# Performance work log

Hardware: AMD Instinct MI355X
Metric: run time of the kernel (lower is better)

Reference implementation:

```python
import jax, jax.numpy as jnp
import numpy as np

B, N, DIM, H, DH = 8, 1024, 512, 8, 64
INNER = H * DH  # 512
G = DH // 4     # SE(3) groups of size 4 per head


def setup_inputs() -> dict:
    key = jax.random.key(0)
    ks = jax.random.split(key, 6)
    x = jax.random.normal(ks[0], (B, N, DIM), jnp.float32)
    rotations = jax.random.normal(ks[1], (B, N, 3, 3), jnp.float32)
    translations = jax.random.normal(ks[2], (B, N, 3), jnp.float32)
    # JaxLinear init: trunc-normal std = 1/sqrt(fan_in), zero bias
    w_qkv = jax.random.normal(ks[3], (DIM, 3 * INNER), jnp.float32) * (1.0 / np.sqrt(DIM))
    b_qkv = jnp.zeros((3 * INNER,), jnp.float32)
    w_out = jax.random.normal(ks[4], (INNER, DIM), jnp.float32) * (1.0 / np.sqrt(INNER))
    b_out = jnp.zeros((DIM,), jnp.float32)
    return {"x": x, "rotations": rotations, "translations": translations,
            "w_qkv": w_qkv, "b_qkv": b_qkv, "w_out": w_out, "b_out": b_out}


def _apply_pose(P, t, transpose):
    # P: [B,N,4,4]; t: [B,H,N,DH] -> reshape to groups of 4 and rotate each group
    tg = t.reshape(B, H, N, G, 4)
    sub = 'bnji,bhncj->bhnci' if transpose else 'bnij,bhncj->bhnci'
    return jnp.einsum(sub, P, tg).reshape(B, H, N, DH)


def reference(x, rotations, translations, w_qkv, b_qkv, w_out, b_out):
    scale = DH ** -0.5
    qkv = x @ w_qkv + b_qkv                      # [B,N,3*INNER]
    q, k, v = jnp.split(qkv, 3, axis=-1)
    to_heads = lambda t: t.reshape(B, N, H, DH).transpose(0, 2, 1, 3)  # b n (h d) -> b h n d
    q, k, v = to_heads(q), to_heads(k), to_heads(v)

    # SE(3) pose matrices
    eye4 = jnp.eye(4, dtype=x.dtype)
    Rt = jnp.swapaxes(rotations, -1, -2)
    t_inv = -jnp.einsum('bnij,bnj->bni', Rt, translations)
    P_qinv = (jnp.broadcast_to(eye4, (B, N, 4, 4))
              .at[..., :3, :3].set(Rt)
              .at[..., :3, 3].set(t_inv))       # inverted query poses
    P_kv = (jnp.broadcast_to(eye4, (B, N, 4, 4))
            .at[..., :3, :3].set(rotations)
            .at[..., :3, 3].set(translations))  # key/value poses

    # per-token rotation of q/k/v (q uses P_qinv^T per original einsum)
    q = _apply_pose(P_qinv, q, transpose=True)
    k = _apply_pose(P_kv, k, transpose=False)
    v = _apply_pose(P_kv, v, transpose=False)   # v_transform=True

    attn = jax.nn.softmax(jnp.einsum('bhqd,bhkd->bhqk', q, k) * scale, axis=-1)
    out = jnp.einsum('bhqk,bhkd->bhqd', attn, v)
    out = _apply_pose(P_qinv, out, transpose=False)  # inverse transform on output

    out = out.transpose(0, 2, 1, 3).reshape(B, N, INNER)  # b h n d -> b n (h d)
    return out @ w_out + b_out
```

## Files before the change

### kernel.cpp

```cpp
#include <hip/hip_runtime.h>
#include <math.h>

#define BSZ   8
#define NSEQ  1024
#define DIM   512
#define NH    8
#define DH    64
#define INNER 512
#define NTOK  (BSZ*NSEQ)
#define QKVN  (3*INNER)

typedef __bf16   bf16x8 __attribute__((ext_vector_type(8)));
typedef _Float16 f16x8  __attribute__((ext_vector_type(8)));
typedef float    f32x4  __attribute__((ext_vector_type(4)));

#define QSCL (0.125f * 1.44269504088896f)

static __device__ __forceinline__ ushort f2bf(float f) {
    union { float f; unsigned u; } v; v.f = f;
    unsigned r = (v.u + 0x7FFFu + ((v.u >> 16) & 1u)) >> 16;
    return (ushort)r;
}
static __device__ __forceinline__ ushort f2h(float f) {
    _Float16 h = (_Float16)f;
    return __builtin_bit_cast(unsigned short, h);
}
static __device__ __forceinline__ void async16(const void* g, void* l) {
    __builtin_amdgcn_global_load_lds(
        (const __attribute__((address_space(1))) unsigned int*)g,
        (__attribute__((address_space(3))) unsigned int*)l, 16, 0, 0);
}

__global__ __launch_bounds__(256) void prep_kernel(
    const float* __restrict__ x,  ushort* __restrict__ xf,
    const float* __restrict__ wq, ushort* __restrict__ wqT,
    const float* __restrict__ wo, ushort* __restrict__ woT)
{
    const int bid = blockIdx.x;
    if (bid < 4096) {
        const int i = bid*256 + threadIdx.x;
        float4 v = ((const float4*)x)[i];
        ushort4 h = { f2h(v.x), f2h(v.y), f2h(v.z), f2h(v.w) };
        ((ushort4*)xf)[i] = h;
        return;
    }
    __shared__ float tile[32][33];
    int K, F, bx, by; const float* in; ushort* outp; int is_q;
    if (bid < 4096 + 768) {
        const int id = bid - 4096;
        bx = id % 48; by = id / 48;
        K = DIM; F = QKVN; in = wq; outp = wqT; is_q = 1;
    } else {
        const int id = bid - 4864;
        bx = id % 16; by = id / 16;
        K = INNER; F = DIM; in = wo; outp = woT; is_q = 0;
    }
    const int lx = threadIdx.x & 31, ly = threadIdx.x >> 5;
#pragma unroll
    for (int u = 0; u < 4; u++) {
        const int k = by*32 + ly + u*8;
        tile[ly + u*8][lx] = in[(size_t)k*F + bx*32 + lx];
    }
    __syncthreads();
#pragma unroll
    for (int u = 0; u < 4; u++) {
        const int f = bx*32 + ly + u*8;
        const float v = tile[lx][ly + u*8];
        outp[(size_t)f*K + by*32 + lx] = is_q ? f2h(v) : f2bf(v);
    }
}

__global__ __launch_bounds__(256) void qkv_gemm_f16(
    const ushort* __restrict__ Ag,
    const ushort* __restrict__ Bg,
    const float* __restrict__ bias, const float* __restrict__ rot,
    const float* __restrict__ trans,
    ushort* __restrict__ qb, ushort* __restrict__ kb, ushort* __restrict__ vt)
{
    extern __shared__ __align__(16) char smem[];

    const int tid  = threadIdx.x;
    const int lane = tid & 63;
    const int w    = tid >> 6;
    const int c    = lane & 15;
    const int quad = lane >> 4;
    const int wr   = w >> 1, wc = w & 1;
    const int tn   = blockIdx.x;
    const int tf   = blockIdx.y;

    f32x4 acc[4][4] = {};

    const int part = w >> 1;
    const int g0   = (w & 1) * 4;
    const ushort* src = (part == 0) ? Ag : Bg;
    const ushort* wbase = src + (size_t)((part == 0 ? tf : tn)*128 + g0*16 + c)*DIM
                          + quad*8;

    auto stage = [&](int k0, int buf) {
#pragma unroll
        for (int g = 0; g < 4; g++)
            async16(wbase + (size_t)g*16*DIM + k0,
                    smem + buf*16384 + part*8192 + (g0 + g)*1024);
    };

    stage(0, 0);
    stage(32, 1);

    for (int ch = 0; ch < 16; ch++) {
        const int cur = ch % 3;
        if (ch < 15) {
            __asm__ volatile("s_waitcnt vmcnt(4)\n\ts_barrier" ::: "memory");
        } else {
            __asm__ volatile("s_waitcnt vmcnt(0)\n\ts_barrier" ::: "memory");
        }
        if (ch < 14) stage((ch+2)*32, (ch+2) % 3);

        const char* B = smem + cur*16384;
        f16x8 fa[4], fb[4];
#pragma unroll
        for (int i = 0; i < 4; i++)
            fa[i] = *(const f16x8*)(B + (wr*4 + i)*1024 + lane*16);
#pragma unroll
        for (int j = 0; j < 4; j++)
            fb[j] = *(const f16x8*)(B + 8192 + (wc*4 + j)*1024 + lane*16);
#pragma unroll
        for (int i = 0; i < 4; i++)
#pragma unroll
            for (int j = 0; j < 4; j++)
                acc[i][j] = __builtin_amdgcn_mfma_f32_16x16x32_f16(
                    fa[i], fb[j], acc[i][j], 0, 0, 0);
    }

    const int sec = tf >> 2;

#pragma unroll
    for (int j = 0; j < 4; j++) {
        const int tc = tn*128 + wc*64 + j*16 + c;
        const int bb = tc >> 10, n = tc & 1023;
        const float* R = rot   + (size_t)(bb*NSEQ + n)*9;
        const float* T = trans + (size_t)(bb*NSEQ + n)*3;
        const float R0=R[0],R1=R[1],R2=R[2],R3=R[3],R4=R[4],R5=R[5],R6=R[6],R7=R[7],R8=R[8];
        const float T0=T[0],T1=T[1],T2=T[2];
        float ti0 = 0.f, ti1 = 0.f, ti2 = 0.f;
        if (sec == 0) {
            ti0 = -(R0*T0 + R3*T1 + R6*T2);
            ti1 = -(R1*T0 + R4*T1 + R7*T2);
            ti2 = -(R2*T0 + R5*T1 + R8*T2);
        }
#pragma unroll
        for (int i = 0; i < 4; i++) {
            const int fr = tf*128 + wr*64 + i*16 + quad*4;
            const int fl = fr & 511;
            const int h  = fl >> 6, d = fl & 63;
            float4 bv = *(const float4*)(bias + fr);
            const float g0v = acc[i][j][0] + bv.x;
            const float g1v = acc[i][j][1] + bv.y;
            const float g2v = acc[i][j][2] + bv.z;
            const float g3v = acc[i][j][3] + bv.w;
            if (sec == 0) {
                float o0 = (R0*g0v + R1*g1v + R2*g2v) * QSCL;
                float o1 = (R3*g0v + R4*g1v + R5*g2v) * QSCL;
                float o2 = (R6*g0v + R7*g1v + R8*g2v) * QSCL;
                float o3 = (ti0*g0v + ti1*g1v + ti2*g2v + g3v) * QSCL;
                ushort4 ov = { f2bf(o0), f2bf(o1), f2bf(o2), f2bf(o3) };
                *(ushort4*)(qb + ((size_t)((bb*NH + h)*NSEQ + n))*DH + d) = ov;
            } else {
                float o0 = R0*g0v + R1*g1v + R2*g2v + T0*g3v;
                float o1 = R3*g0v + R4*g1v + R5*g2v + T1*g3v;
                float o2 = R6*g0v + R7*g1v + R8*g2v + T2*g3v;
                float o3 = g3v;
                if (sec == 1) {
                    ushort4 ov = { f2bf(o0), f2bf(o1), f2bf(o2), f2bf(o3) };
                    *(ushort4*)(kb + ((size_t)((bb*NH + h)*NSEQ + n))*DH + d) = ov;
                } else {
                    ushort* vtb = vt + ((size_t)(bb*NH + h)*DH + d)*NSEQ + n;
                    vtb[0*NSEQ] = f2bf(o0);
                    vtb[1*NSEQ] = f2bf(o1);
                    vtb[2*NSEQ] = f2bf(o2);
                    vtb[3*NSEQ] = f2bf(o3);
                }
            }
        }
    }
}

__global__ __launch_bounds__(256, 2) void attn_mfma_kernel(
    const ushort* __restrict__ qb, const ushort* __restrict__ kb,
    const ushort* __restrict__ vt, const float* __restrict__ rot,
    const float* __restrict__ trans, ushort* __restrict__ om)
{
    __shared__ __align__(16) char smem[58368];

    const int tid  = threadIdx.x;
    const int lane = tid & 63;
    const int w    = tid >> 6;
    const int c    = lane & 15;
    const int quad = lane >> 4;

    const int o   = blockIdx.x;
    const int wid = (o & 7) * 128 + (o >> 3);
    const int qt  = wid & 15;
    const int bh  = wid >> 4;
    const int bb = bh >> 3, h = bh & 7;

    const ushort* Q = qb + (size_t)bh * NSEQ * DH;
    const ushort* K = kb + (size_t)bh * NSEQ * DH;
    const ushort* V = vt + (size_t)bh * DH * NSEQ;

    bf16x8 qf[2];
    {
        const ushort* qrow = Q + (size_t)(qt*64 + w*16 + c)*DH + quad*8;
        qf[0] = *(const bf16x8*)(qrow);
        qf[1] = *(const bf16x8*)(qrow + 32);
    }

    f32x4 Oacc[4] = {};
    float lsum[4] = {};

    auto stage = [&](int kt, int buf) {
#pragma unroll
        for (int u = 0; u < 2; u++) {
            const int seg = w + u*4;
            const int nt = seg >> 1, hh = seg & 1;
            const ushort* g = K + (size_t)(kt*64 + nt*16 + c)*DH + hh*32 + quad*8;
            async16(g, smem + buf*16384 + seg*1024);
        }
#pragma unroll
        for (int u = 0; u < 2; u++) {
            const int s2 = w + u*4;
            const int nt = s2 >> 1, kc = s2 & 1;
            const ushort* g = V + (size_t)(nt*16 + c)*NSEQ + kt*64 + kc*32 + quad*8;
            async16(g, smem + buf*16384 + 8192 + s2*1024);
        }
    };

    stage(0, 0);
    stage(1, 1);

    ushort (*Psw)[72] = (ushort (*)[72])(smem + 49152 + w*2304);

    for (int kt = 0; kt < 16; kt++) {
        const int cur = kt % 3;
        if (kt < 15) {
            __asm__ volatile("s_waitcnt vmcnt(4)\n\ts_barrier" ::: "memory");
        } else {
            __asm__ volatile("s_waitcnt vmcnt(0)\n\ts_barrier" ::: "memory");
        }
        if (kt < 14) stage(kt + 2, (kt + 2) % 3);

        const char* Kb = smem + cur*16384;
        const char* Vb = smem + cur*16384 + 8192;

        f32x4 s[4];
#pragma unroll
        for (int nt = 0; nt < 4; nt++) {
            bf16x8 k0 = *(const bf16x8*)(Kb + (nt*2+0)*1024 + lane*16);
            bf16x8 k1 = *(const bf16x8*)(Kb + (nt*2+1)*1024 + lane*16);
            f32x4 a = {0.f, 0.f, 0.f, 0.f};
            a = __builtin_amdgcn_mfma_f32_16x16x32_bf16(qf[0], k0, a, 0, 0, 0);
            a = __builtin_amdgcn_mfma_f32_16x16x32_bf16(qf[1], k1, a, 0, 0, 0);
            s[nt] = a;
        }

#pragma unroll
        for (int nt = 0; nt < 4; nt++)
#pragma unroll
            for (int r = 0; r < 4; r++) {
                const float p = exp2f(s[nt][r]);
                lsum[r] += p;
                Psw[quad*4 + r][nt*16 + c] = (ushort)__builtin_bit_cast(
                    unsigned short, (__bf16)p);
            }
        __asm__ volatile("s_waitcnt lgkmcnt(0)" ::: "memory");

#pragma unroll
        for (int kc2 = 0; kc2 < 2; kc2++) {
            bf16x8 vfr[4];
#pragma unroll
            for (int nt = 0; nt < 4; nt++)
                vfr[nt] = *(const bf16x8*)(Vb + (nt*2+kc2)*1024 + lane*16);
            bf16x8 a = *(const bf16x8*)&Psw[c][kc2*32 + quad*8];
#pragma unroll
            for (int nt = 0; nt < 4; nt++)
                Oacc[nt] = __builtin_amdgcn_mfma_f32_16x16x32_bf16(
                    a, vfr[nt], Oacc[nt], 0, 0, 0);
        }
    }

#pragma unroll
    for (int mk = 1; mk < 16; mk <<= 1)
#pragma unroll
        for (int r = 0; r < 4; r++)
            lsum[r] += __shfl_xor(lsum[r], mk);

    __syncthreads();
    float (*Osh)[68] = (float (*)[68])smem;
    {
        float inv[4];
#pragma unroll
        for (int r = 0; r < 4; r++) inv[r] = 1.f / lsum[r];
#pragma unroll
        for (int nt = 0; nt < 4; nt++)
#pragma unroll
            for (int r = 0; r < 4; r++)
                Osh[w*16 + quad*4 + r][nt*16 + c] = Oacc[nt][r] * inv[r];
    }
    __syncthreads();

#pragma unroll
    for (int u = 0; u < 4; u++) {
        const int t   = tid + u*256;
        const int row = t >> 4;
        const int g   = t & 15;
        const int n   = qt*64 + row;
        const float o0 = Osh[row][g*4+0], o1 = Osh[row][g*4+1];
        const float o2 = Osh[row][g*4+2], o3 = Osh[row][g*4+3];
        const float* R = rot   + (size_t)(bb*NSEQ + n)*9;
        const float* T = trans + (size_t)(bb*NSEQ + n)*3;
        const float ti0 = -(R[0]*T[0] + R[3]*T[1] + R[6]*T[2]);
        const float ti1 = -(R[1]*T[0] + R[4]*T[1] + R[7]*T[2]);
        const float ti2 = -(R[2]*T[0] + R[5]*T[1] + R[8]*T[2]);
        const float p0 = R[0]*o0 + R[3]*o1 + R[6]*o2 + ti0*o3;
        const float p1 = R[1]*o0 + R[4]*o1 + R[7]*o2 + ti1*o3;
        const float p2 = R[2]*o0 + R[5]*o1 + R[8]*o2 + ti2*o3;
        const float p3 = o3;
        ushort4 hv = { f2bf(p0), f2bf(p1), f2bf(p2), f2bf(p3) };
        *(ushort4*)(om + (size_t)(bb*NSEQ + n)*INNER + h*DH + g*4) = hv;
    }
}

__global__ __launch_bounds__(256) void out_gemm_mfma(
    const ushort* __restrict__ Ag, const ushort* __restrict__ Bg,
    const float* __restrict__ bias, float* __restrict__ out)
{
    extern __shared__ __align__(16) char smem[];

    const int tid  = threadIdx.x;
    const int lane = tid & 63;
    const int w    = tid >> 6;
    const int c    = lane & 15;
    const int quad = lane >> 4;
    const int wr   = w >> 1, wc = w & 1;
    const int tn   = blockIdx.x;
    const int tf   = blockIdx.y;

    f32x4 acc[4][4] = {};

    const int part = w >> 1;
    const int g0   = (w & 1) * 4;
    const ushort* src = (part == 0) ? Ag : Bg;
    const ushort* wbase = src + (size_t)((part == 0 ? tf : tn)*128 + g0*16 + c)*INNER
                          + quad*8;

    auto stage = [&](int k0, int buf) {
#pragma unroll
        for (int g = 0; g < 4; g++)
            async16(wbase + (size_t)g*16*INNER + k0,
                    smem + buf*16384 + part*8192 + (g0 + g)*1024);
    };

    stage(0, 0);
    stage(32, 1);
    stage(64, 2);

    for (int ch = 0; ch < 16; ch++) {
        const int cur = ch & 3;
        if (ch < 14) {
            __asm__ volatile("s_waitcnt vmcnt(8)\n\ts_barrier" ::: "memory");
        } else if (ch == 14) {
            __asm__ volatile("s_waitcnt vmcnt(4)\n\ts_barrier" ::: "memory");
        } else {
            __asm__ volatile("s_waitcnt vmcnt(0)\n\ts_barrier" ::: "memory");
        }
        if (ch < 13) stage((ch+3)*32, (ch+3) & 3);

        const char* B = smem + cur*16384;
        bf16x8 fa[4], fb[4];
#pragma unroll
        for (int i = 0; i < 4; i++)
            fa[i] = *(const bf16x8*)(B + (wr*4 + i)*1024 + lane*16);
#pragma unroll
        for (int j = 0; j < 4; j++)
            fb[j] = *(const bf16x8*)(B + 8192 + (wc*4 + j)*1024 + lane*16);
#pragma unroll
        for (int i = 0; i < 4; i++)
#pragma unroll
            for (int j = 0; j < 4; j++)
                acc[i][j] = __builtin_amdgcn_mfma_f32_16x16x32_bf16(
                    fa[i], fb[j], acc[i][j], 0, 0, 0);
    }

#pragma unroll
    for (int j = 0; j < 4; j++) {
        const int tc = tn*128 + wc*64 + j*16 + c;
#pragma unroll
        for (int i = 0; i < 4; i++) {
            const int fr = tf*128 + wr*64 + i*16 + quad*4;
            float4 bv = *(const float4*)(bias + fr);
            float4 ov = { acc[i][j][0] + bv.x, acc[i][j][1] + bv.y,
                          acc[i][j][2] + bv.z, acc[i][j][3] + bv.w };
            *(float4*)(out + (size_t)tc*DIM + fr) = ov;
        }
    }
}

extern "C" void kernel_launch(void* const* d_in, const int* in_sizes, int n_in,
                              void* d_out, int out_size, void* d_ws, size_t ws_size,
                              hipStream_t stream) {
    (void)in_sizes; (void)n_in; (void)out_size; (void)ws_size;
    const float* x     = (const float*)d_in[0];
    const float* rot   = (const float*)d_in[1];
    const float* trans = (const float*)d_in[2];
    const float* w_qkv = (const float*)d_in[3];
    const float* b_qkv = (const float*)d_in[4];
    const float* w_out = (const float*)d_in[5];
    const float* b_out = (const float*)d_in[6];
    float* out = (float*)d_out;

    const size_t HB = (size_t)BSZ*NH*NSEQ*DH;
    ushort* qb   = (ushort*)d_ws;
    ushort* kb   = qb   + HB;
    ushort* vt   = kb   + HB;
    ushort* woTh = vt   + HB;
    ushort* wqTh = woTh + (size_t)DIM*INNER;
    ushort* xf   = wqTh + (size_t)QKVN*DIM;
    ushort* om   = xf;

    static int s_attr_done = 0;
    if (!s_attr_done) {
        (void)hipFuncSetAttribute((const void*)out_gemm_mfma,
            hipFuncAttributeMaxDynamicSharedMemorySize, 65536);
        s_attr_done = 1;
    }

    prep_kernel<<<dim3(5120), 256, 0, stream>>>(
        x, xf, w_qkv, wqTh, w_out, woTh);

    qkv_gemm_f16<<<dim3(NTOK/128, QKVN/128), 256, 49152, stream>>>(
        wqTh, xf, b_qkv, rot, trans, qb, kb, vt);
    attn_mfma_kernel<<<dim3(1024), 256, 0, stream>>>(
        qb, kb, vt, rot, trans, om);
    out_gemm_mfma<<<dim3(NTOK/128, DIM/128), 256, 65536, stream>>>(
        woTh, om, b_out, out);
}
```

Before: 168.4 us.

## Shrink GEMM shared-memory footprints to raise occupancy; halve out-GEMM feature tile

The QKV GEMM drops from a 3-stage to a 2-stage LDS ring (32KB instead of 48KB) and adds an extra barrier after each chunk's MFMAs so a buffer is not overwritten while still being read. The output GEMM now uses 64x128 tiles with 2x4 accumulators per wave, which doubles the grid. It keeps a 4-deep ring of 12KB stages (48KB total), removes the dynamic-shared-memory attribute call, and adds launch_bounds(…,2). The aim is more resident blocks per CU and better latency hiding. The costs are less prefetch depth, an extra barrier per iteration in the QKV GEMM, and more redundant B-tile loads in the output GEMM.

```diff
diff --git a/kernel.cpp b/kernel.cpp
--- a/kernel.cpp
+++ b/kernel.cpp
@@ -104,16 +104,15 @@
     };
 
     stage(0, 0);
-    stage(32, 1);
 
     for (int ch = 0; ch < 16; ch++) {
-        const int cur = ch % 3;
+        const int cur = ch & 1, nxt = cur ^ 1;
         if (ch < 15) {
+            stage((ch+1)*32, nxt);
             __asm__ volatile("s_waitcnt vmcnt(4)\n\ts_barrier" ::: "memory");
         } else {
             __asm__ volatile("s_waitcnt vmcnt(0)\n\ts_barrier" ::: "memory");
         }
-        if (ch < 14) stage((ch+2)*32, (ch+2) % 3);
 
         const char* B = smem + cur*16384;
         f16x8 fa[4], fb[4];
@@ -129,6 +128,7 @@
             for (int j = 0; j < 4; j++)
                 acc[i][j] = __builtin_amdgcn_mfma_f32_16x16x32_f16(
                     fa[i], fb[j], acc[i][j], 0, 0, 0);
+        __asm__ volatile("s_waitcnt lgkmcnt(0)\n\ts_barrier" ::: "memory");
     }
 
     const int sec = tf >> 2;
@@ -329,7 +329,7 @@
     }
 }
 
-__global__ __launch_bounds__(256) void out_gemm_mfma(
+__global__ __launch_bounds__(256, 2) void out_gemm_mfma(
     const ushort* __restrict__ Ag, const ushort* __restrict__ Bg,
     const float* __restrict__ bias, float* __restrict__ out)
 {
@@ -344,19 +344,23 @@
     const int tn   = blockIdx.x;
     const int tf   = blockIdx.y;
 
-    f32x4 acc[4][4] = {};
-
-    const int part = w >> 1;
-    const int g0   = (w & 1) * 4;
-    const ushort* src = (part == 0) ? Ag : Bg;
-    const ushort* wbase = src + (size_t)((part == 0 ? tf : tn)*128 + g0*16 + c)*INNER
-                          + quad*8;
+    f32x4 acc[2][4] = {};
 
     auto stage = [&](int k0, int buf) {
 #pragma unroll
-        for (int g = 0; g < 4; g++)
-            async16(wbase + (size_t)g*16*INNER + k0,
-                    smem + buf*16384 + part*8192 + (g0 + g)*1024);
+        for (int g = 0; g < 3; g++) {
+            const int s = w*3 + g;
+            const ushort* src;
+            int dst;
+            if (s < 4) {
+                src = Ag + (size_t)(tf*64 + s*16 + c)*INNER + k0 + quad*8;
+                dst = buf*12288 + s*1024;
+            } else {
+                src = Bg + (size_t)(tn*128 + (s-4)*16 + c)*INNER + k0 + quad*8;
+                dst = buf*12288 + 4096 + (s-4)*1024;
+            }
+            async16(src, smem + dst);
+        }
     };
 
     stage(0, 0);
@@ -365,25 +369,25 @@
 
     for (int ch = 0; ch < 16; ch++) {
         const int cur = ch & 3;
-        if (ch < 14) {
-            __asm__ volatile("s_waitcnt vmcnt(8)\n\ts_barrier" ::: "memory");
+        if (ch <= 13) {
+            __asm__ volatile("s_waitcnt vmcnt(6)\n\ts_barrier" ::: "memory");
         } else if (ch == 14) {
-            __asm__ volatile("s_waitcnt vmcnt(4)\n\ts_barrier" ::: "memory");
+            __asm__ volatile("s_waitcnt vmcnt(3)\n\ts_barrier" ::: "memory");
         } else {
             __asm__ volatile("s_waitcnt vmcnt(0)\n\ts_barrier" ::: "memory");
         }
         if (ch < 13) stage((ch+3)*32, (ch+3) & 3);
 
-        const char* B = smem + cur*16384;
-        bf16x8 fa[4], fb[4];
-#pragma unroll
-        for (int i = 0; i < 4; i++)
-            fa[i] = *(const bf16x8*)(B + (wr*4 + i)*1024 + lane*16);
+        const char* B = smem + cur*12288;
+        bf16x8 fa[2], fb[4];
+#pragma unroll
+        for (int i = 0; i < 2; i++)
+            fa[i] = *(const bf16x8*)(B + (wr*2 + i)*1024 + lane*16);
 #pragma unroll
         for (int j = 0; j < 4; j++)
-            fb[j] = *(const bf16x8*)(B + 8192 + (wc*4 + j)*1024 + lane*16);
-#pragma unroll
-        for (int i = 0; i < 4; i++)
+            fb[j] = *(const bf16x8*)(B + 4096 + (wc*4 + j)*1024 + lane*16);
+#pragma unroll
+        for (int i = 0; i < 2; i++)
 #pragma unroll
             for (int j = 0; j < 4; j++)
                 acc[i][j] = __builtin_amdgcn_mfma_f32_16x16x32_bf16(
@@ -394,8 +398,8 @@
     for (int j = 0; j < 4; j++) {
         const int tc = tn*128 + wc*64 + j*16 + c;
 #pragma unroll
-        for (int i = 0; i < 4; i++) {
-            const int fr = tf*128 + wr*64 + i*16 + quad*4;
+        for (int i = 0; i < 2; i++) {
+            const int fr = tf*64 + wr*32 + i*16 + quad*4;
             float4 bv = *(const float4*)(bias + fr);
             float4 ov = { acc[i][j][0] + bv.x, acc[i][j][1] + bv.y,
                           acc[i][j][2] + bv.z, acc[i][j][3] + bv.w };
@@ -426,20 +430,13 @@
     ushort* xf   = wqTh + (size_t)QKVN*DIM;
     ushort* om   = xf;
 
-    static int s_attr_done = 0;
-    if (!s_attr_done) {
-        (void)hipFuncSetAttribute((const void*)out_gemm_mfma,
-            hipFuncAttributeMaxDynamicSharedMemorySize, 65536);
-        s_attr_done = 1;
-    }
-
     prep_kernel<<<dim3(5120), 256, 0, stream>>>(
         x, xf, w_qkv, wqTh, w_out, woTh);
 
-    qkv_gemm_f16<<<dim3(NTOK/128, QKVN/128), 256, 49152, stream>>>(
+    qkv_gemm_f16<<<dim3(NTOK/128, QKVN/128), 256, 32768, stream>>>(
         wqTh, xf, b_qkv, rot, trans, qb, kb, vt);
     attn_mfma_kernel<<<dim3(1024), 256, 0, stream>>>(
         qb, kb, vt, rot, trans, om);
-    out_gemm_mfma<<<dim3(NTOK/128, DIM/128), 256, 65536, stream>>>(
+    out_gemm_mfma<<<dim3(NTOK/128, DIM/64), 256, 49152, stream>>>(
         woTh, om, b_out, out);
 }
```

New measurement: 170.6 us. Within noise of the previous version (+1.3%).
